# Performance work log

Measured on AMD Instinct MI355X. Metric: run time of the kernel, lower is better.

## Reference

```python
import jax, jax.numpy as jnp
import numpy as np
import heapq
from collections import defaultdict

V = 50257   # vocab_size
D = 512     # embedding_dim
B = 4096    # batch of (embedding, target) samples


def _build_paths(freqs):
    """Huffman tree exactly as in HierarchicalSoftmax.build_tree; returns padded path arrays."""
    heap = [[w, [n]] for n, w in freqs.items()]
    heapq.heapify(heap)
    tree = defaultdict(list)
    while len(heap) > 1:
        lo = heapq.heappop(heap)
        hi = heapq.heappop(heap)
        for node in lo[1]:
            tree[node].append((len(heap), 0))
        for node in hi[1]:
            tree[node].append((len(heap), 1))
        heapq.heappush(heap, [lo[0] + hi[0], lo[1] + hi[1]])
    n_leaves = len(freqs)
    L = max(len(tree[v]) for v in range(n_leaves))  # max path length (~27 for zipf)
    nodes = np.zeros((n_leaves, L), dtype=np.int32)
    dirs = np.zeros((n_leaves, L), dtype=np.int32)
    mask = np.zeros((n_leaves, L), dtype=bool)
    for v in range(n_leaves):
        for i, (p, d) in enumerate(tree[v]):
            nodes[v, i] = p
            dirs[v, i] = d
            mask[v, i] = True
    return nodes, dirs, mask


def setup_inputs() -> dict:
    key = jax.random.key(0)
    k1, k2, k3 = jax.random.split(key, 3)
    freqs = {i: 1.0 / (i + 1) for i in range(V)}  # deterministic zipf frequencies
    nodes, dirs, mask = _build_paths(freqs)
    embeddings = jax.random.normal(k1, (B, D), dtype=jnp.float32)
    # one Linear(D,1) per internal node: V-1 internal nodes total
    W = jax.random.normal(k2, (V - 1, D), dtype=jnp.float32) * (1.0 / np.sqrt(D))
    b = jnp.zeros((V - 1,), dtype=jnp.float32)
    target = jax.random.randint(k3, (B,), 0, V)
    return {
        "embeddings": embeddings,
        "W": W,
        "b": b,
        "target": target,
        "path_nodes": jnp.asarray(nodes),
        "path_dirs": jnp.asarray(dirs),
        "path_mask": jnp.asarray(mask),
    }


def reference(embeddings, W, b, target, path_nodes, path_dirs, path_mask):
    # Gather each sample's root-to-leaf path of internal-node classifiers.
    nodes = path_nodes[target]          # [B, L]
    dirs = path_dirs[target]            # [B, L]
    mask = path_mask[target]            # [B, L] bool
    Wg = W[nodes]                       # [B, L, D] gathered classifier rows
    scores = jnp.einsum('bld,bd->bl', Wg, embeddings) + b[nodes]  # [B, L]
    # direction==1 -> sigmoid(s); direction==0 -> 1 - sigmoid(s) == sigmoid(-s)
    signed = jnp.where(dirs == 1, scores, -scores)
    factors = jnp.where(mask, jax.nn.sigmoid(signed), 1.0)
    return jnp.prod(factors, axis=-1)   # [B] path probabilities
```

## Files before the change

### kernel.cpp

```cpp
#include <hip/hip_runtime.h>


#define HS_D 512

__global__ __launch_bounds__(256) void hs_kernel(
    const float* __restrict__ emb,
    const float* __restrict__ W,
    const float* __restrict__ bias,
    const int*   __restrict__ target,
    const int*   __restrict__ nodes,
    const int*   __restrict__ dirs,
    float*       __restrict__ out,
    int B, int L)
{
    const int wid  = blockIdx.x * (blockDim.x >> 6) + (threadIdx.x >> 6);
    const int lane = threadIdx.x & 63;
    if (wid >= B) return;

    const float4* e4 = (const float4*)(emb + (size_t)wid * HS_D);
    const float4 e0 = e4[lane];
    const float4 e1 = e4[lane + 64];

    const int t = __builtin_amdgcn_readfirstlane(target[wid]);
    const int* __restrict__ nrow = nodes + (size_t)t * L;
    const int* __restrict__ drow = dirs  + (size_t)t * L;

    float prod = 1.0f;
    for (int l = 0; l < L; ++l) {
        const int node = __builtin_amdgcn_readfirstlane(nrow[l]);
        const int dir  = __builtin_amdgcn_readfirstlane(drow[l]);

        const float4* w4 = (const float4*)(W + (size_t)node * HS_D);
        const float4 w0 = w4[lane];
        const float4 w1 = w4[lane + 64];

        float p = e0.x*w0.x + e0.y*w0.y + e0.z*w0.z + e0.w*w0.w
                + e1.x*w1.x + e1.y*w1.y + e1.z*w1.z + e1.w*w1.w;
        #pragma unroll
        for (int m = 32; m > 0; m >>= 1) p += __shfl_xor(p, m, 64);

        const float s  = p + bias[node];
        const float sg = (dir != 0) ? s : -s;
        prod *= 1.0f / (1.0f + __expf(-sg));

        if (node == 0) break;
    }

    if (lane == 0) out[wid] = prod;
}

extern "C" void kernel_launch(void* const* d_in, const int* in_sizes, int n_in,
                              void* d_out, int out_size, void* d_ws, size_t ws_size,
                              hipStream_t stream)
{
    const float* emb    = (const float*)d_in[0];
    const float* W      = (const float*)d_in[1];
    const float* bias   = (const float*)d_in[2];
    const int*   target = (const int*)  d_in[3];
    const int*   nodes  = (const int*)  d_in[4];
    const int*   dirs   = (const int*)  d_in[5];
    float*       out    = (float*)d_out;

    const int B = in_sizes[3];
    const int V = in_sizes[2] + 1;
    const int L = in_sizes[4] / V;

    const int wavesPerBlock = 4;
    const int grid = (B + wavesPerBlock - 1) / wavesPerBlock;
    hs_kernel<<<grid, 256, 0, stream>>>(emb, W, bias, target, nodes, dirs, out, B, L);
}
```

Measured before the change: 166.7 us.

## Preload path indices per wave and unroll path loop by four

Each wave now loads the whole path of node indices and directions in one vector load, then uses ballots to get the path length and a direction bitmask. This replaces the dependent scalar loads and the per-step early exit. The main loop is unrolled by four, so four W row gathers and four shuffle reductions are in flight together, which is meant to hide gather latency. It also switches to fmaf chains and a hardware reciprocal for the sigmoid, which slightly changes rounding and raises register use.

```diff
diff --git a/kernel.cpp b/kernel.cpp
--- a/kernel.cpp
+++ b/kernel.cpp
@@ -2,6 +2,24 @@
 
 
 #define HS_D 512
+
+__device__ __forceinline__ float dot8(const float4 e0, const float4 e1,
+                                      const float4 a, const float4 b) {
+    float p;
+    p = e0.x * a.x;
+    p = fmaf(e0.y, a.y, p);
+    p = fmaf(e0.z, a.z, p);
+    p = fmaf(e0.w, a.w, p);
+    p = fmaf(e1.x, b.x, p);
+    p = fmaf(e1.y, b.y, p);
+    p = fmaf(e1.z, b.z, p);
+    p = fmaf(e1.w, b.w, p);
+    return p;
+}
+
+__device__ __forceinline__ float fast_sigmoid(float s) {
+    return __builtin_amdgcn_rcpf(1.0f + __expf(-s));
+}
 
 __global__ __launch_bounds__(256) void hs_kernel(
     const float* __restrict__ emb,
@@ -22,28 +40,71 @@
     const float4 e1 = e4[lane + 64];
 
     const int t = __builtin_amdgcn_readfirstlane(target[wid]);
-    const int* __restrict__ nrow = nodes + (size_t)t * L;
-    const int* __restrict__ drow = dirs  + (size_t)t * L;
+
+    int nval = 0, dval = 0;
+    if (lane < L) {
+        nval = nodes[(size_t)t * L + lane];
+        dval = dirs [(size_t)t * L + lane];
+    }
+    const unsigned long long rootmask = __ballot(lane < L && nval == 0);
+    const int plen = __ffsll((long long)rootmask);
+    const unsigned long long dirmask = __ballot(dval != 0);
 
     float prod = 1.0f;
-    for (int l = 0; l < L; ++l) {
-        const int node = __builtin_amdgcn_readfirstlane(nrow[l]);
-        const int dir  = __builtin_amdgcn_readfirstlane(drow[l]);
+    int l = 0;
 
-        const float4* w4 = (const float4*)(W + (size_t)node * HS_D);
-        const float4 w0 = w4[lane];
-        const float4 w1 = w4[lane + 64];
+    for (; l + 4 <= plen; l += 4) {
+        const int n0 = __builtin_amdgcn_readfirstlane(__shfl(nval, l + 0, 64));
+        const int n1 = __builtin_amdgcn_readfirstlane(__shfl(nval, l + 1, 64));
+        const int n2 = __builtin_amdgcn_readfirstlane(__shfl(nval, l + 2, 64));
+        const int n3 = __builtin_amdgcn_readfirstlane(__shfl(nval, l + 3, 64));
 
-        float p = e0.x*w0.x + e0.y*w0.y + e0.z*w0.z + e0.w*w0.w
-                + e1.x*w1.x + e1.y*w1.y + e1.z*w1.z + e1.w*w1.w;
+        const float4* w0 = (const float4*)(W + (size_t)n0 * HS_D);
+        const float4* w1 = (const float4*)(W + (size_t)n1 * HS_D);
+        const float4* w2 = (const float4*)(W + (size_t)n2 * HS_D);
+        const float4* w3 = (const float4*)(W + (size_t)n3 * HS_D);
+
+        const float4 a0 = w0[lane], b0 = w0[lane + 64];
+        const float4 a1 = w1[lane], b1 = w1[lane + 64];
+        const float4 a2 = w2[lane], b2 = w2[lane + 64];
+        const float4 a3 = w3[lane], b3 = w3[lane + 64];
+
+        float p0 = dot8(e0, e1, a0, b0);
+        float p1 = dot8(e0, e1, a1, b1);
+        float p2 = dot8(e0, e1, a2, b2);
+        float p3 = dot8(e0, e1, a3, b3);
+
+        #pragma unroll
+        for (int m = 32; m > 0; m >>= 1) {
+            p0 += __shfl_xor(p0, m, 64);
+            p1 += __shfl_xor(p1, m, 64);
+            p2 += __shfl_xor(p2, m, 64);
+            p3 += __shfl_xor(p3, m, 64);
+        }
+
+        float s0 = p0 + bias[n0];
+        float s1 = p1 + bias[n1];
+        float s2 = p2 + bias[n2];
+        float s3 = p3 + bias[n3];
+        s0 = ((dirmask >> (l + 0)) & 1ull) ? s0 : -s0;
+        s1 = ((dirmask >> (l + 1)) & 1ull) ? s1 : -s1;
+        s2 = ((dirmask >> (l + 2)) & 1ull) ? s2 : -s2;
+        s3 = ((dirmask >> (l + 3)) & 1ull) ? s3 : -s3;
+
+        prod *= fast_sigmoid(s0) * fast_sigmoid(s1)
+              * fast_sigmoid(s2) * fast_sigmoid(s3);
+    }
+
+    for (; l < plen; ++l) {
+        const int n = __builtin_amdgcn_readfirstlane(__shfl(nval, l, 64));
+        const float4* w = (const float4*)(W + (size_t)n * HS_D);
+        const float4 a = w[lane], b = w[lane + 64];
+        float p = dot8(e0, e1, a, b);
         #pragma unroll
         for (int m = 32; m > 0; m >>= 1) p += __shfl_xor(p, m, 64);
-
-        const float s  = p + bias[node];
-        const float sg = (dir != 0) ? s : -s;
-        prod *= 1.0f / (1.0f + __expf(-sg));
-
-        if (node == 0) break;
+        float s = p + bias[n];
+        s = ((dirmask >> l) & 1ull) ? s : -s;
+        prod *= fast_sigmoid(s);
     }
 
     if (lane == 0) out[wid] = prod;
```

Measured after the change: 163.0 us. -2.2%, faster.
